# Kernel optimization log

Measured on AMD Instinct MI355X. Metric: run time of the kernel, lower is better.

Reference implementation:

```python
import jax, jax.numpy as jnp
import numpy as np


def _causal_conv(x, w, b, dilation):
    # x: (B, Cin, N), w: (Cout, Cin, K) -> causal: left-pad (K-1)*dilation
    pad = (w.shape[-1] - 1) * dilation
    y = jax.lax.conv_general_dilated(
        x, w, window_strides=(1,), padding=[(pad, 0)],
        rhs_dilation=(dilation,), dimension_numbers=('NCH', 'OIH', 'NCH'))
    return y + b[None, :, None]


def setup_inputs() -> dict:
    key = jax.random.key(0)
    ks = jax.random.split(key, 8)
    B, N, C, L = 8, 32768, 16, 30
    s = 0.1  # weight scale to avoid gate saturation
    return {
        'x': jax.random.normal(ks[0], (B, N), dtype=jnp.float32) * 1000.0,  # int16-like samples
        'lengths': jax.random.randint(ks[1], (B,), N // 2, N),
        'w0': jax.random.normal(ks[2], (C, 1, 2), dtype=jnp.float32) * s,
        'b0': jnp.zeros((C,), jnp.float32),
        'wf': jax.random.normal(ks[3], (L - 1, C, C, 2), dtype=jnp.float32) * s,
        'bf': jnp.zeros((L - 1, C), jnp.float32),
        'wg': jax.random.normal(ks[4], (L - 1, C, C, 2), dtype=jnp.float32) * s,
        'bg': jnp.zeros((L - 1, C), jnp.float32),
        'wa': jax.random.normal(ks[5], (64, C), dtype=jnp.float32) * s,
        'ba': jnp.zeros((64,), jnp.float32),
        'wo': jax.random.normal(ks[6], (256, 64), dtype=jnp.float32) * s,
        'bo': jnp.zeros((256,), jnp.float32),
    }


def reference(x, lengths, w0, b0, wf, bf, wg, bg, wa, ba, wo, bo):
    L = wf.shape[0] + 1  # total layers (layer 0 is plain causal conv)
    xin = (x / 32768.0)[:, None, :]            # (B,1,N), int16 normalization 65536/2
    out0 = _causal_conv(xin, w0, b0, 1)        # (B,C,N)
    agg = out0                                 # skip aggregate
    h = xin + out0                             # residual input (broadcast 1->C channels)
    for i in range(1, L):                      # fixed small layer count
        d = 2 ** (i % 10)
        f = _causal_conv(h, wf[i - 1], bf[i - 1], d)
        g = _causal_conv(h, wg[i - 1], bg[i - 1], d)
        out = jnp.tanh(f) * jax.nn.sigmoid(g)  # gated activation unit
        agg = agg + out
        h = h + out
    a = jnp.einsum('oc,bcn->bon', wa, jax.nn.relu(agg)) + ba[None, :, None]  # agregate1x1
    o = jnp.einsum('oc,bcn->bon', wo, jax.nn.relu(a)) + bo[None, :, None]    # output1x1
    o = jax.nn.log_softmax(o, axis=1)
    mask = (jnp.arange(o.shape[-1]) < lengths[:, None]).astype(o.dtype)      # (B,N)
    return o * mask[:, None, :]
```

## Files before the change

### kernel.cpp

```cpp
#include <hip/hip_runtime.h>

#define NSEQ 32768
#define NB 8
#define NC 16
#define LBLK 1024
#define LPX (LBLK / 8)
#define QGRD 4096
#define QPX (QGRD / 8)

typedef float vfloat4 __attribute__((ext_vector_type(4)));

__device__ __forceinline__ float sigm_f(float x) {
    return __fdividef(1.f, 1.f + __expf(-x));
}
__device__ __forceinline__ float tanh_f(float x) {
    return __fdividef(2.f, 1.f + __expf(-2.f * x)) - 1.f;
}

__device__ __forceinline__ void nt_store4(float* p, float a, float b, float c, float d) {
    vfloat4 v; v.x = a; v.y = b; v.z = c; v.w = d;
    __builtin_nontemporal_store(v, (vfloat4*)p);
}

__global__ __launch_bounds__(256) void k_layer0(
    const float* __restrict__ x, const float* __restrict__ w0,
    const float* __restrict__ b0, float* __restrict__ h)
{
    int bid = blockIdx.x;
    int tid = ((bid & 7) * LPX + (bid >> 3)) * 256 + threadIdx.x;
    int n = tid & (NSEQ - 1);
    const float inv = 1.f / 32768.f;
    float xc = x[tid] * inv;
    float xp = (n >= 1) ? x[tid - 1] * inv : 0.f;
    float v[NC];
#pragma unroll
    for (int c = 0; c < NC; c++) {
        float o = w0[c * 2] * xp + w0[c * 2 + 1] * xc + b0[c];
        v[c] = xc + o;
    }
    float* ph = h + (size_t)tid * NC;
#pragma unroll
    for (int i = 0; i < 4; i++)
        nt_store4(ph + i * 4, v[i * 4], v[i * 4 + 1], v[i * 4 + 2], v[i * 4 + 3]);
}

__global__ __launch_bounds__(256) void k_layer(
    const float* __restrict__ hin, float* __restrict__ hout,
    const float* __restrict__ wf, const float* __restrict__ bf,
    const float* __restrict__ wg, const float* __restrict__ bg, int d)
{
    int bid = blockIdx.x;
    int lbid = (bid & 7) * QPX + (bid >> 3);
    int t = threadIdx.x;
    int pos = lbid * 64 + (t & 63);
    int q = __builtin_amdgcn_readfirstlane(t >> 6);
    int n = pos & (NSEQ - 1);

    float hc[NC], hp[NC];
    {
        const float4* pc = (const float4*)(hin + (size_t)pos * NC);
#pragma unroll
        for (int i = 0; i < 4; i++) {
            float4 tv = pc[i];
            hc[i * 4] = tv.x; hc[i * 4 + 1] = tv.y; hc[i * 4 + 2] = tv.z; hc[i * 4 + 3] = tv.w;
        }
    }
    if (n >= d) {
        const float4* pp = (const float4*)(hin + (size_t)(pos - d) * NC);
#pragma unroll
        for (int i = 0; i < 4; i++) {
            float4 tv = pp[i];
            hp[i * 4] = tv.x; hp[i * 4 + 1] = tv.y; hp[i * 4 + 2] = tv.z; hp[i * 4 + 3] = tv.w;
        }
    } else {
#pragma unroll
        for (int i = 0; i < NC; i++) hp[i] = 0.f;
    }

    const int c0 = q * 4;
    float f[4], g[4];
#pragma unroll
    for (int j = 0; j < 4; j++) { f[j] = bf[c0 + j]; g[j] = bg[c0 + j]; }

#pragma unroll
    for (int ci = 0; ci < NC; ci++) {
        float xp = hp[ci], xc = hc[ci];
#pragma unroll
        for (int j = 0; j < 4; j++) {
            int co = c0 + j;
            f[j] = fmaf(wf[(co * NC + ci) * 2 + 0], xp, f[j]);
            f[j] = fmaf(wf[(co * NC + ci) * 2 + 1], xc, f[j]);
            g[j] = fmaf(wg[(co * NC + ci) * 2 + 0], xp, g[j]);
            g[j] = fmaf(wg[(co * NC + ci) * 2 + 1], xc, g[j]);
        }
    }

    float v[4];
#pragma unroll
    for (int j = 0; j < 4; j++) {
        float outv = tanh_f(f[j]) * sigm_f(g[j]);
        v[j] = hc[c0 + j] + outv;
    }
    nt_store4(hout + (size_t)pos * NC + c0, v[0], v[1], v[2], v[3]);
}

__global__ __launch_bounds__(512, 2) void k_final(
    const float* __restrict__ hfin, const float* __restrict__ x,
    const int* __restrict__ lengths,
    const float* __restrict__ wa, const float* __restrict__ ba,
    const float* __restrict__ wo, const float* __restrict__ bo,
    float* __restrict__ out)
{
    __shared__ float s_r[64][17];
    __shared__ float s_ra[64][65];
    __shared__ float s_red[2][8][64];

    int t = threadIdx.x;
    int p = t & 63;
    int q = __builtin_amdgcn_readfirstlane(t >> 6);
    int blk = blockIdx.x;
    int b = blk >> 9;
    int n0 = (blk & 511) << 6;
    int n = n0 + p;
    size_t pos = (size_t)b * NSEQ + n;
    float xin = x[pos] * (1.f / 32768.f);

    if (q < 4) {
        const float4* ph = (const float4*)(hfin + pos * NC);
        float4 v = ph[q];
        s_r[p][q * 4 + 0] = fmaxf(v.x - xin, 0.f);
        s_r[p][q * 4 + 1] = fmaxf(v.y - xin, 0.f);
        s_r[p][q * 4 + 2] = fmaxf(v.z - xin, 0.f);
        s_r[p][q * 4 + 3] = fmaxf(v.w - xin, 0.f);
    }
    __syncthreads();

    {
        float r[NC];
#pragma unroll
        for (int c = 0; c < NC; c++) r[c] = s_r[p][c];
#pragma unroll
        for (int jj = 0; jj < 8; jj++) {
            int j = q * 8 + jj;
            float acc = ba[j];
#pragma unroll
            for (int c = 0; c < NC; c++) acc = fmaf(wa[j * NC + c], r[c], acc);
            s_ra[p][j] = fmaxf(acc, 0.f);
        }
    }
    __syncthreads();

    float ra[64];
#pragma unroll
    for (int j = 0; j < 64; j++) ra[j] = s_ra[p][j];

    float o[32];
    float m = -1e30f;
#pragma unroll 4
    for (int kk = 0; kk < 32; kk++) {
        int k = q * 32 + kk;
        float acc = bo[k];
#pragma unroll
        for (int j = 0; j < 64; j++) acc = fmaf(wo[k * 64 + j], ra[j], acc);
        o[kk] = acc;
        m = fmaxf(m, acc);
    }
    s_red[0][q][p] = m;
    __syncthreads();
    m = fmaxf(fmaxf(fmaxf(s_red[0][0][p], s_red[0][1][p]),
                    fmaxf(s_red[0][2][p], s_red[0][3][p])),
              fmaxf(fmaxf(s_red[0][4][p], s_red[0][5][p]),
                    fmaxf(s_red[0][6][p], s_red[0][7][p])));
    float s = 0.f;
#pragma unroll
    for (int kk = 0; kk < 32; kk++) s += __expf(o[kk] - m);
    s_red[1][q][p] = s;
    __syncthreads();
    s = ((s_red[1][0][p] + s_red[1][1][p]) + (s_red[1][2][p] + s_red[1][3][p]))
      + ((s_red[1][4][p] + s_red[1][5][p]) + (s_red[1][6][p] + s_red[1][7][p]));
    float lse = m + __logf(s);

    bool valid = n < lengths[b];
    float* po = out + ((size_t)b * 256 + q * 32) * NSEQ + n;
#pragma unroll
    for (int kk = 0; kk < 32; kk++) {
        float v = valid ? (o[kk] - lse) : 0.f;
        __builtin_nontemporal_store(v, &po[(size_t)kk * NSEQ]);
    }
}

extern "C" void kernel_launch(void* const* d_in, const int* in_sizes, int n_in,
                              void* d_out, int out_size, void* d_ws, size_t ws_size,
                              hipStream_t stream) {
    const float* x   = (const float*)d_in[0];
    const int* lens  = (const int*)d_in[1];
    const float* w0  = (const float*)d_in[2];
    const float* b0  = (const float*)d_in[3];
    const float* wf  = (const float*)d_in[4];
    const float* bf  = (const float*)d_in[5];
    const float* wg  = (const float*)d_in[6];
    const float* bg  = (const float*)d_in[7];
    const float* wa  = (const float*)d_in[8];
    const float* ba  = (const float*)d_in[9];
    const float* wo  = (const float*)d_in[10];
    const float* bo  = (const float*)d_in[11];
    float* out = (float*)d_out;

    float* hA = (float*)d_ws;
    float* hB = hA + (size_t)NB * NSEQ * NC;

    k_layer0<<<dim3(LBLK), dim3(256), 0, stream>>>(x, w0, b0, hA);

    float* cur = hA;
    float* nxt = hB;
    for (int i = 1; i <= 29; i++) {
        int d = 1 << (i % 10);
        k_layer<<<dim3(QGRD), dim3(256), 0, stream>>>(cur, nxt,
                                         wf + (size_t)(i - 1) * NC * NC * 2,
                                         bf + (size_t)(i - 1) * NC,
                                         wg + (size_t)(i - 1) * NC * NC * 2,
                                         bg + (size_t)(i - 1) * NC, d);
        float* tmp = cur; cur = nxt; nxt = tmp;
    }

    dim3 fgrd(NB * (NSEQ / 64));
    k_final<<<fgrd, dim3(512), 0, stream>>>(cur, x, lens, wa, ba, wo, bo, out);
}
```

Measured before the change: 615.7 us.

## Stage output weights in LDS and widen final kernel to 1024 threads

The final projection kernel now copies the 256x64 output weight matrix into shared memory per block and reads it from LDS instead of global/scalar loads. The block grows to 1024 threads (16 waves), each computing 16 of the 256 logits, with the softmax reductions extended to 16 partials. The layer kernel also gets an occupancy hint of 6 blocks per CU. The 64KB weight copy per block adds load traffic and LDS pressure that may limit occupancy of the final kernel.

Result: slower. 669.9 us (+8.8%).

```diff
diff --git a/kernel.cpp b/kernel.cpp
--- a/kernel.cpp
+++ b/kernel.cpp
@@ -44,7 +44,7 @@
         nt_store4(ph + i * 4, v[i * 4], v[i * 4 + 1], v[i * 4 + 2], v[i * 4 + 3]);
 }
 
-__global__ __launch_bounds__(256) void k_layer(
+__global__ __launch_bounds__(256, 6) void k_layer(
     const float* __restrict__ hin, float* __restrict__ hout,
     const float* __restrict__ wf, const float* __restrict__ bf,
     const float* __restrict__ wg, const float* __restrict__ bg, int d)
@@ -104,16 +104,17 @@
     nt_store4(hout + (size_t)pos * NC + c0, v[0], v[1], v[2], v[3]);
 }
 
-__global__ __launch_bounds__(512, 2) void k_final(
+__global__ __launch_bounds__(1024, 1) void k_final(
     const float* __restrict__ hfin, const float* __restrict__ x,
     const int* __restrict__ lengths,
     const float* __restrict__ wa, const float* __restrict__ ba,
     const float* __restrict__ wo, const float* __restrict__ bo,
     float* __restrict__ out)
 {
+    __shared__ float s_wo[256 * 64];
     __shared__ float s_r[64][17];
     __shared__ float s_ra[64][65];
-    __shared__ float s_red[2][8][64];
+    __shared__ float s_red[2][16][64];
 
     int t = threadIdx.x;
     int p = t & 63;
@@ -125,6 +126,16 @@
     size_t pos = (size_t)b * NSEQ + n;
     float xin = x[pos] * (1.f / 32768.f);
 
+    {
+        const float4* src = (const float4*)wo;
+        float4* dst = (float4*)s_wo;
+#pragma unroll
+        for (int i = 0; i < 4; i++) {
+            int idx = t + i * 1024;
+            dst[idx] = src[idx];
+        }
+    }
+
     if (q < 4) {
         const float4* ph = (const float4*)(hfin + pos * NC);
         float4 v = ph[q];
@@ -140,8 +151,8 @@
 #pragma unroll
         for (int c = 0; c < NC; c++) r[c] = s_r[p][c];
 #pragma unroll
-        for (int jj = 0; jj < 8; jj++) {
-            int j = q * 8 + jj;
+        for (int jj = 0; jj < 4; jj++) {
+            int j = q * 4 + jj;
             float acc = ba[j];
 #pragma unroll
             for (int c = 0; c < NC; c++) acc = fmaf(wa[j * NC + c], r[c], acc);
@@ -154,36 +165,44 @@
 #pragma unroll
     for (int j = 0; j < 64; j++) ra[j] = s_ra[p][j];
 
-    float o[32];
+    float o[16];
     float m = -1e30f;
-#pragma unroll 4
-    for (int kk = 0; kk < 32; kk++) {
-        int k = q * 32 + kk;
+#pragma unroll 2
+    for (int kk = 0; kk < 16; kk++) {
+        int k = q * 16 + kk;
         float acc = bo[k];
-#pragma unroll
-        for (int j = 0; j < 64; j++) acc = fmaf(wo[k * 64 + j], ra[j], acc);
+        const float* wrow = s_wo + k * 64;
+#pragma unroll
+        for (int j = 0; j < 64; j++) acc = fmaf(wrow[j], ra[j], acc);
         o[kk] = acc;
         m = fmaxf(m, acc);
     }
     s_red[0][q][p] = m;
     __syncthreads();
-    m = fmaxf(fmaxf(fmaxf(s_red[0][0][p], s_red[0][1][p]),
-                    fmaxf(s_red[0][2][p], s_red[0][3][p])),
-              fmaxf(fmaxf(s_red[0][4][p], s_red[0][5][p]),
-                    fmaxf(s_red[0][6][p], s_red[0][7][p])));
+    m = fmaxf(
+        fmaxf(fmaxf(fmaxf(s_red[0][0][p],  s_red[0][1][p]),
+                    fmaxf(s_red[0][2][p],  s_red[0][3][p])),
+              fmaxf(fmaxf(s_red[0][4][p],  s_red[0][5][p]),
+                    fmaxf(s_red[0][6][p],  s_red[0][7][p]))),
+        fmaxf(fmaxf(fmaxf(s_red[0][8][p],  s_red[0][9][p]),
+                    fmaxf(s_red[0][10][p], s_red[0][11][p])),
+              fmaxf(fmaxf(s_red[0][12][p], s_red[0][13][p]),
+                    fmaxf(s_red[0][14][p], s_red[0][15][p]))));
     float s = 0.f;
 #pragma unroll
-    for (int kk = 0; kk < 32; kk++) s += __expf(o[kk] - m);
+    for (int kk = 0; kk < 16; kk++) s += __expf(o[kk] - m);
     s_red[1][q][p] = s;
     __syncthreads();
-    s = ((s_red[1][0][p] + s_red[1][1][p]) + (s_red[1][2][p] + s_red[1][3][p]))
-      + ((s_red[1][4][p] + s_red[1][5][p]) + (s_red[1][6][p] + s_red[1][7][p]));
+    s = (((s_red[1][0][p]  + s_red[1][1][p])  + (s_red[1][2][p]  + s_red[1][3][p]))
+       + ((s_red[1][4][p]  + s_red[1][5][p])  + (s_red[1][6][p]  + s_red[1][7][p])))
+      + (((s_red[1][8][p]  + s_red[1][9][p])  + (s_red[1][10][p] + s_red[1][11][p]))
+       + ((s_red[1][12][p] + s_red[1][13][p]) + (s_red[1][14][p] + s_red[1][15][p])));
     float lse = m + __logf(s);
 
     bool valid = n < lengths[b];
-    float* po = out + ((size_t)b * 256 + q * 32) * NSEQ + n;
-#pragma unroll
-    for (int kk = 0; kk < 32; kk++) {
+    float* po = out + ((size_t)b * 256 + q * 16) * NSEQ + n;
+#pragma unroll
+    for (int kk = 0; kk < 16; kk++) {
         float v = valid ? (o[kk] - lse) : 0.f;
         __builtin_nontemporal_store(v, &po[(size_t)kk * NSEQ]);
     }
@@ -224,5 +243,5 @@
     }
 
     dim3 fgrd(NB * (NSEQ / 64));
-    k_final<<<fgrd, dim3(512), 0, stream>>>(cur, x, lens, wa, ba, wo, bo, out);
-}
+    k_final<<<fgrd, dim3(1024), 0, stream>>>(cur, x, lens, wa, ba, wo, bo, out);
+}
```
